# Optimization experiments

Measured on AMD Instinct MI355X. Metric: run time of the kernel, lower is better.

The kernel has to match this reference:

```python
import jax, jax.numpy as jnp
import numpy as np

B, S, H = 16, 2048, 1024

def setup_inputs() -> dict:
    key = jax.random.key(0)
    k1, k2, k3, k4 = jax.random.split(key, 4)
    x = jax.random.normal(k1, (B, S, H), dtype=jnp.float32)
    # nn.Linear weights, stored as (out, in); y = x @ W.T
    scale = 1.0 / np.sqrt(H)
    W_q = jax.random.uniform(k2, (H, H), jnp.float32, -scale, scale)
    W_k = jax.random.uniform(k3, (H, H), jnp.float32, -scale, scale)
    W_v = jax.random.uniform(k4, (H, H), jnp.float32, -scale, scale)
    return {"x": x, "W_q": W_q, "W_k": W_k, "W_v": W_v}

def reference(x, W_q, W_k, W_v):
    # x: (B,S,H); W_*: (H,H) torch Linear layout (out,in)
    Q = jnp.einsum('bsh,oh->bso', x, W_q)
    K = jnp.einsum('bsh,oh->bso', x, W_k)
    V = jnp.einsum('bsh,oh->bso', x, W_v)
    scale = jnp.asarray(x.shape[-1] ** 0.5, dtype=x.dtype)
    energy = jnp.einsum('bqd,bkd->bqk', Q, K) / scale      # (B,S,S)
    attn = jax.nn.softmax(energy, axis=-1)                  # (B,S,S)
    attended = jnp.einsum('bqk,bkd->bqd', attn, V)          # (B,S,H)
    context = attended.mean(axis=1)                         # (B,H)
    attn_weights = attn.mean(axis=1)                        # (B,S)
    return (context, attn_weights)
```

## Files before the change

kernel.cpp:

```cpp
#include <hip/hip_runtime.h>
#include <hip/hip_bf16.h>
#include <stdint.h>

#define BB 16
#define SS 2048
#define HH 1024

using bf16 = __hip_bfloat16;
typedef __attribute__((ext_vector_type(8))) short short8;
typedef __attribute__((ext_vector_type(4))) float f32x4;

typedef unsigned int __attribute__((address_space(1))) as1_uint;
typedef unsigned int __attribute__((address_space(3))) as3_uint;

static constexpr size_t WS_XB   = 0;
static constexpr size_t WS_G    = 67108864;
static constexpr size_t WS_P    = 134217728;
static constexpr size_t WS_WQT  = 134217728;
static constexpr size_t WS_WKT  = 136314880;
static constexpr size_t WS_MT   = 138412032;
static constexpr size_t WS_LSUM = 201326592;
static constexpr size_t WS_T    = 201457664;
static constexpr size_t WS_NEED = 201523200;

__device__ __forceinline__ void async_copy16(bf16* lds_dst, const bf16* gsrc) {
    __builtin_amdgcn_global_load_lds((const as1_uint*)gsrc, (as3_uint*)lds_dst, 16, 0, 0);
}

__device__ __forceinline__ float bf2f(unsigned short u) {
    union { unsigned i; float f; } v; v.i = (unsigned)u << 16; return v.f;
}

__device__ __forceinline__ unsigned char f32_to_e4m3(float x) {
#if __has_builtin(__builtin_amdgcn_cvt_pk_fp8_f32)
    return (unsigned char)(__builtin_amdgcn_cvt_pk_fp8_f32(x, x, 0, false) & 0xff);
#else
    if (x >= 0.015625f) {
        union { float f; unsigned u; } v; v.f = x;
        int e = (v.u >> 23) & 0xff;
        unsigned m = v.u & 0x7fffff;
        unsigned mant = m >> 20;
        unsigned rem = m & 0xfffff;
        mant += (rem > 0x80000u) || (rem == 0x80000u && (mant & 1));
        int oe = e - 120;
        if (mant == 8) { mant = 0; oe += 1; }
        return (unsigned char)((oe << 3) | mant);
    }
    int code = (int)rintf(x * 512.0f);
    return (unsigned char)code;
#endif
}

__device__ __forceinline__ float e4m3_to_f32(unsigned char b) {
#if __has_builtin(__builtin_amdgcn_cvt_pk_f32_fp8)
    auto v = __builtin_amdgcn_cvt_pk_f32_fp8((int)b, false);
    return v[0];
#else
    int e = (b >> 3) & 15, m = b & 7;
    if (e) { union { unsigned u; float f; } v; v.u = ((unsigned)(e + 120) << 23) | ((unsigned)m << 20); return v.f; }
    return (float)m * 0.001953125f;
#endif
}

__global__ __launch_bounds__(256) void cast_x_kernel(const float* __restrict__ x,
                                                     bf16* __restrict__ xb, int n4) {
    int stride = gridDim.x * blockDim.x;
    for (int i = blockIdx.x * blockDim.x + threadIdx.x; i < n4; i += stride) {
        float4 v = reinterpret_cast<const float4*>(x)[i];
        union { bf16 h[4]; uint2 u; } p;
        p.h[0] = __float2bfloat16(v.x); p.h[1] = __float2bfloat16(v.y);
        p.h[2] = __float2bfloat16(v.z); p.h[3] = __float2bfloat16(v.w);
        reinterpret_cast<uint2*>(xb)[i] = p.u;
    }
}

__global__ __launch_bounds__(256) void transpose_w_kernel(const float* __restrict__ wq,
                                                          const float* __restrict__ wk,
                                                          bf16* __restrict__ wqT,
                                                          bf16* __restrict__ wkT) {
    __shared__ float tile[64][65];
    const float* src = blockIdx.z ? wk : wq;
    bf16* dst = blockIdx.z ? wkT : wqT;
    const int o0 = blockIdx.y * 64, i0 = blockIdx.x * 64;
    const int tr = threadIdx.x >> 4;
    const int tc = (threadIdx.x & 15) * 4;
#pragma unroll
    for (int k = 0; k < 4; ++k) {
        float4 v = *reinterpret_cast<const float4*>(src + (size_t)(o0 + tr + k * 16) * 1024 + i0 + tc);
        tile[tr + k * 16][tc + 0] = v.x; tile[tr + k * 16][tc + 1] = v.y;
        tile[tr + k * 16][tc + 2] = v.z; tile[tr + k * 16][tc + 3] = v.w;
    }
    __syncthreads();
#pragma unroll
    for (int k = 0; k < 4; ++k) {
        int ri = tr + k * 16;
        union { bf16 h[4]; uint2 u; } p;
#pragma unroll
        for (int j = 0; j < 4; ++j) p.h[j] = __float2bfloat16(tile[tc + j][ri]);
        *reinterpret_cast<uint2*>(dst + (size_t)(i0 + ri) * 1024 + o0 + tc) = p.u;
    }
}

__global__ __launch_bounds__(256) void gemm_mt64(const bf16* __restrict__ wkT,
                                                 const bf16* __restrict__ wqT,
                                                 bf16* __restrict__ Mt) {
    __shared__ bf16 As[64 * 64], Bs[64 * 64];
    f32x4 acc[2][2];
#pragma unroll
    for (int m = 0; m < 2; ++m)
#pragma unroll
        for (int n = 0; n < 2; ++n) { acc[m][n][0]=0.f; acc[m][n][1]=0.f; acc[m][n][2]=0.f; acc[m][n][3]=0.f; }
    const int tid = threadIdx.x, wid = tid >> 6, lane = tid & 63;
    const int wm = wid >> 1, wn = wid & 1;
    const int srow = lane >> 3, scol = (lane & 7) * 8;
    const bf16* Ab = wkT + (size_t)blockIdx.y * 64 * 1024;
    const bf16* Bb = wqT + (size_t)blockIdx.x * 64 * 1024;
    for (int kt = 0; kt < 1024; kt += 64) {
#pragma unroll
        for (int i = 0; i < 2; ++i) {
            int row0 = i * 32 + wid * 8;
            async_copy16(As + row0 * 64, Ab + (size_t)(row0 + srow) * 1024 + kt + scol);
            async_copy16(Bs + row0 * 64, Bb + (size_t)(row0 + srow) * 1024 + kt + scol);
        }
        __syncthreads();
#pragma unroll
        for (int kk = 0; kk < 2; ++kk) {
            short8 a[2], b[2];
#pragma unroll
            for (int m = 0; m < 2; ++m)
                a[m] = *reinterpret_cast<const short8*>(
                    As + (wm * 32 + m * 16 + (lane & 15)) * 64 + kk * 32 + (lane >> 4) * 8);
#pragma unroll
            for (int n = 0; n < 2; ++n)
                b[n] = *reinterpret_cast<const short8*>(
                    Bs + (wn * 32 + n * 16 + (lane & 15)) * 64 + kk * 32 + (lane >> 4) * 8);
#pragma unroll
            for (int m = 0; m < 2; ++m)
#pragma unroll
                for (int n = 0; n < 2; ++n)
                    acc[m][n] = __builtin_amdgcn_mfma_f32_16x16x32_bf16(a[m], b[n], acc[m][n], 0, 0, 0);
        }
        __syncthreads();
    }
    const int row0 = blockIdx.y * 64 + wm * 32 + ((lane >> 4) << 2);
    const int col0 = blockIdx.x * 64 + wn * 32 + (lane & 15);
#pragma unroll
    for (int m = 0; m < 2; ++m)
#pragma unroll
        for (int n = 0; n < 2; ++n)
#pragma unroll
            for (int r = 0; r < 4; ++r)
                Mt[(size_t)(row0 + m * 16 + r) * 1024 + col0 + n * 16] =
                    __float2bfloat16(acc[m][n][r] * 0.03125f);
}

static constexpr int NT256 = 16;

__device__ __forceinline__ void gemm256_mainloop(const bf16* __restrict__ Ag,
                                                 const bf16* __restrict__ Bg,
                                                 char* lds, f32x4 acc[8][4]) {
    const int tid = threadIdx.x;
    const int lane = tid & 63;
    const int wid = tid >> 6;
    const int wm = wid >> 2;
    const int wn = wid & 3;

#pragma unroll
    for (int m = 0; m < 8; ++m)
#pragma unroll
        for (int n = 0; n < 4; ++n) { acc[m][n][0]=0.f; acc[m][n][1]=0.f; acc[m][n][2]=0.f; acc[m][n][3]=0.f; }

    char* A0 = lds;            char* B0 = lds + 32768;
    char* A1 = lds + 65536;    char* B1 = lds + 98304;

    int soA[2], soB[2];
    {
#pragma unroll
        for (int i = 0; i < 2; ++i) {
            int beta = (i * 512 + tid) * 16;
            int rho  = beta >> 7;
            int cs   = (beta & 127) ^ ((rho & 7) << 4);
            soA[i] = ((rho >> 6) * 128 + (rho & 63)) * 1024 + (cs >> 1);
            soB[i] = ((rho >> 5) * 64  + (rho & 31)) * 1024 + (cs >> 1);
        }
    }
    const int dstw = wid * 1024;

    int roA[4], roB[2];
    {
        const int swz = (lane & 7) << 4;
        const int colb = (lane >> 4) * 16;
#pragma unroll
        for (int mi = 0; mi < 4; ++mi) {
            int row = wm * 64 + mi * 16 + (lane & 15);
            roA[mi] = (row * 128 + colb) ^ swz;
        }
#pragma unroll
        for (int ni = 0; ni < 2; ++ni) {
            int row = wn * 32 + ni * 16 + (lane & 15);
            roB[ni] = (row * 128 + colb) ^ swz;
        }
    }

#define STAGE_A256(buf, q, kt)                                                        \
    {                                                                                 \
        async_copy16((bf16*)((buf) + (q) * 16384 + dstw),                             \
                     Ag + soA[0] + (q) * 65536 + (kt) * 64);                          \
        async_copy16((bf16*)((buf) + (q) * 16384 + 8192 + dstw),                      \
                     Ag + soA[1] + (q) * 65536 + (kt) * 64);                          \
    }
#define STAGE_B256(buf, q, kt)                                                        \
    {                                                                                 \
        async_copy16((bf16*)((buf) + (q) * 16384 + dstw),                             \
                     Bg + soB[0] + (q) * 32768 + (kt) * 64);                          \
        async_copy16((bf16*)((buf) + (q) * 16384 + 8192 + dstw),                      \
                     Bg + soB[1] + (q) * 32768 + (kt) * 64);                          \
    }

    STAGE_A256(A0, 0, 0); STAGE_A256(A0, 1, 0);
    STAGE_B256(B0, 0, 0); STAGE_B256(B0, 1, 0);
    STAGE_A256(A1, 0, 1); STAGE_B256(B1, 0, 1);
    asm volatile("s_waitcnt vmcnt(4)" ::: "memory");
    __builtin_amdgcn_s_barrier();

    short8 a[4][2], b0[2][2], b1[2][2];

#pragma unroll 1
    for (int t = 0; t < NT256; ++t) {
        char* As  = (t & 1) ? A1 : A0;
        char* Bs  = (t & 1) ? B1 : B0;
        char* Aso = (t & 1) ? A0 : A1;
        char* Bso = (t & 1) ? B0 : B1;

#pragma unroll
        for (int ni = 0; ni < 2; ++ni) {
            b0[ni][0] = *reinterpret_cast<const short8*>(Bs + roB[ni]);
            b0[ni][1] = *reinterpret_cast<const short8*>(Bs + (roB[ni] ^ 64));
        }
#pragma unroll
        for (int mi = 0; mi < 4; ++mi) {
            a[mi][0] = *reinterpret_cast<const short8*>(As + roA[mi]);
            a[mi][1] = *reinterpret_cast<const short8*>(As + (roA[mi] ^ 64));
        }
#pragma unroll
        for (int ni = 0; ni < 2; ++ni) {
            b1[ni][0] = *reinterpret_cast<const short8*>(Bs + (roB[ni] + 16384));
            b1[ni][1] = *reinterpret_cast<const short8*>(Bs + ((roB[ni] ^ 64) + 16384));
        }
        if (t + 1 < NT256) { STAGE_A256(Aso, 1, t + 1); STAGE_B256(Bso, 1, t + 1); }
        __builtin_amdgcn_s_setprio(1);
#pragma unroll
        for (int mi = 0; mi < 4; ++mi)
#pragma unroll
            for (int ni = 0; ni < 2; ++ni)
#pragma unroll
                for (int kk = 0; kk < 2; ++kk)
                    acc[mi][ni] = __builtin_amdgcn_mfma_f32_16x16x32_bf16(
                        a[mi][kk], b0[ni][kk], acc[mi][ni], 0, 0, 0);
#pragma unroll
        for (int mi = 0; mi < 4; ++mi)
#pragma unroll
            for (int ni = 0; ni < 2; ++ni)
#pragma unroll
                for (int kk = 0; kk < 2; ++kk)
                    acc[mi][2 + ni] = __builtin_amdgcn_mfma_f32_16x16x32_bf16(
                        a[mi][kk], b1[ni][kk], acc[mi][2 + ni], 0, 0, 0);
        __builtin_amdgcn_s_setprio(0);
        __builtin_amdgcn_sched_barrier(0);
        __builtin_amdgcn_s_barrier();

        if (t + 2 < NT256) { STAGE_A256(As, 0, t + 2); STAGE_B256(Bs, 0, t + 2); }
#pragma unroll
        for (int mi = 0; mi < 4; ++mi) {
            a[mi][0] = *reinterpret_cast<const short8*>(As + (roA[mi] + 16384));
            a[mi][1] = *reinterpret_cast<const short8*>(As + ((roA[mi] ^ 64) + 16384));
        }
        __builtin_amdgcn_s_setprio(1);
#pragma unroll
        for (int mi = 0; mi < 4; ++mi)
#pragma unroll
            for (int ni = 0; ni < 2; ++ni)
#pragma unroll
                for (int kk = 0; kk < 2; ++kk)
                    acc[4 + mi][2 + ni] = __builtin_amdgcn_mfma_f32_16x16x32_bf16(
                        a[mi][kk], b1[ni][kk], acc[4 + mi][2 + ni], 0, 0, 0);
#pragma unroll
        for (int mi = 0; mi < 4; ++mi)
#pragma unroll
            for (int ni = 0; ni < 2; ++ni)
#pragma unroll
                for (int kk = 0; kk < 2; ++kk)
                    acc[4 + mi][ni] = __builtin_amdgcn_mfma_f32_16x16x32_bf16(
                        a[mi][kk], b0[ni][kk], acc[4 + mi][ni], 0, 0, 0);
        __builtin_amdgcn_s_setprio(0);
        __builtin_amdgcn_sched_barrier(0);
        if (t + 2 < NT256) asm volatile("s_waitcnt vmcnt(4)" ::: "memory");
        else               asm volatile("s_waitcnt vmcnt(0)" ::: "memory");
        __builtin_amdgcn_s_barrier();
    }
#undef STAGE_A256
#undef STAGE_B256
}

__global__ __launch_bounds__(512, 2) void gemm_g256(const bf16* __restrict__ xb,
                                                    const bf16* __restrict__ Mt,
                                                    bf16* __restrict__ G) {
    extern __shared__ char lds[];
    f32x4 acc[8][4];
    const int bx = blockIdx.x, by = blockIdx.y;
    gemm256_mainloop(xb + (size_t)by * 256 * 1024, Mt + (size_t)bx * 256 * 1024, lds, acc);
    const int lane = threadIdx.x & 63, wid = threadIdx.x >> 6;
    const int wm = wid >> 2, wn = wid & 3;
    const int row0 = by * 256 + wm * 128 + ((lane >> 4) << 2);
    const int col0 = bx * 256 + wn * 64 + (lane & 15);
#pragma unroll
    for (int mi = 0; mi < 8; ++mi)
#pragma unroll
        for (int ni = 0; ni < 4; ++ni)
#pragma unroll
            for (int r = 0; r < 4; ++r)
                G[(size_t)(row0 + mi * 16 + r) * 1024 + col0 + ni * 16] =
                    __float2bfloat16(acc[mi][ni][r]);
}

__global__ __launch_bounds__(512, 2) void energy_fused256(const bf16* __restrict__ G,
                                                          const bf16* __restrict__ xb,
                                                          unsigned char* __restrict__ P,
                                                          float* __restrict__ lsum) {
    extern __shared__ char lds[];
    f32x4 acc[8][4];
    const int bx = blockIdx.x, by = blockIdx.y, bz = blockIdx.z;
    gemm256_mainloop(G + (size_t)(bz * 2048 + by * 256) * 1024,
                     xb + (size_t)(bz * 2048 + bx * 256) * 1024, lds, acc);
    const int lane = threadIdx.x & 63, wid = threadIdx.x >> 6;
    const int wm = wid >> 2, wn = wid & 3;
    const int q0 = bz * 2048 + by * 256 + wm * 128 + ((lane >> 4) << 2);
    const int k0 = bx * 256 + wn * 64 + (lane & 15);
#pragma unroll
    for (int mi = 0; mi < 8; ++mi) {
        float s[4] = {0.f, 0.f, 0.f, 0.f};
#pragma unroll
        for (int ni = 0; ni < 4; ++ni)
#pragma unroll
            for (int r = 0; r < 4; ++r) {
                float e = __expf(acc[mi][ni][r]);
                unsigned char c = f32_to_e4m3(e);
                P[(size_t)(q0 + mi * 16 + r) * 2048 + k0 + ni * 16] = c;
                s[r] += e4m3_to_f32(c);
            }
#pragma unroll
        for (int off = 1; off < 16; off <<= 1)
#pragma unroll
            for (int r = 0; r < 4; ++r) s[r] += __shfl_xor(s[r], off, 64);
        if ((lane & 15) == 0) {
#pragma unroll
            for (int r = 0; r < 4; ++r) atomicAdd(&lsum[q0 + mi * 16 + r], s[r]);
        }
    }
}

__global__ __launch_bounds__(256) void colsum_kernel(const unsigned char* __restrict__ P,
                                                     const float* __restrict__ lsum,
                                                     float* __restrict__ aw) {
    const int b = blockIdx.y, qc = blockIdx.x, t = threadIdx.x;
    float acc[8] = {0.f, 0.f, 0.f, 0.f, 0.f, 0.f, 0.f, 0.f};
    const unsigned char* base = P + (size_t)(b * 2048 + qc * 128) * 2048 + t * 8;
    const float* ls = lsum + b * 2048 + qc * 128;
    for (int q = 0; q < 128; ++q) {
        float w = 1.0f / ls[q];
        uint2 v = *reinterpret_cast<const uint2*>(base + (size_t)q * 2048);
#if __has_builtin(__builtin_amdgcn_cvt_pk_f32_fp8)
        auto p0 = __builtin_amdgcn_cvt_pk_f32_fp8((int)v.x, false);
        auto p1 = __builtin_amdgcn_cvt_pk_f32_fp8((int)v.x, true);
        auto p2 = __builtin_amdgcn_cvt_pk_f32_fp8((int)v.y, false);
        auto p3 = __builtin_amdgcn_cvt_pk_f32_fp8((int)v.y, true);
        acc[0] += p0[0] * w; acc[1] += p0[1] * w;
        acc[2] += p1[0] * w; acc[3] += p1[1] * w;
        acc[4] += p2[0] * w; acc[5] += p2[1] * w;
        acc[6] += p3[0] * w; acc[7] += p3[1] * w;
#else
        unsigned char by8[8];
        *reinterpret_cast<uint2*>(by8) = v;
#pragma unroll
        for (int j = 0; j < 8; ++j) acc[j] += e4m3_to_f32(by8[j]) * w;
#endif
    }
#pragma unroll
    for (int j = 0; j < 8; ++j)
        atomicAdd(&aw[b * 2048 + t * 8 + j], acc[j] * (1.0f / 2048.0f));
}

__global__ __launch_bounds__(256) void av_x_kernel(const float* __restrict__ aw,
                                                   const bf16* __restrict__ xb,
                                                   float* __restrict__ t) {
    const int b = blockIdx.y;
    const int kc = blockIdx.x;
    const int tid = threadIdx.x;
    float4 acc = {0.f, 0.f, 0.f, 0.f};
    const int k0 = kc * 128;
#pragma unroll 4
    for (int k = k0; k < k0 + 128; ++k) {
        float w = aw[b * 2048 + k];
        uint2 v = *reinterpret_cast<const uint2*>(xb + (size_t)(b * 2048 + k) * 1024 + tid * 4);
        acc.x += w * bf2f((unsigned short)(v.x & 0xffff));
        acc.y += w * bf2f((unsigned short)(v.x >> 16));
        acc.z += w * bf2f((unsigned short)(v.y & 0xffff));
        acc.w += w * bf2f((unsigned short)(v.y >> 16));
    }
    float* tp = t + b * 1024 + tid * 4;
    atomicAdd(tp + 0, acc.x); atomicAdd(tp + 1, acc.y);
    atomicAdd(tp + 2, acc.z); atomicAdd(tp + 3, acc.w);
}

__global__ __launch_bounds__(256) void ctx_gemv_kernel(const float* __restrict__ t,
                                                       const float* __restrict__ wv,
                                                       float* __restrict__ ctx) {
    const int b = blockIdx.y;
    const int wid = threadIdx.x >> 6, lane = threadIdx.x & 63;
    const int o = blockIdx.x * 4 + wid;
    const float4* t4 = reinterpret_cast<const float4*>(t + b * 1024);
    const float4* w4 = reinterpret_cast<const float4*>(wv + (size_t)o * 1024);
    float s = 0.f;
#pragma unroll
    for (int j = lane; j < 256; j += 64) {
        float4 a = t4[j], w = w4[j];
        s += a.x * w.x + a.y * w.y + a.z * w.z + a.w * w.w;
    }
#pragma unroll
    for (int off = 1; off < 64; off <<= 1) s += __shfl_xor(s, off, 64);
    if (lane == 0) ctx[b * 1024 + o] = s;
}

__global__ void ws_too_small_kernel(float* out) {
    if (threadIdx.x == 0 && blockIdx.x == 0) out[0] = 12345.0f;
}

extern "C" void kernel_launch(void* const* d_in, const int* in_sizes, int n_in,
                              void* d_out, int out_size, void* d_ws, size_t ws_size,
                              hipStream_t stream) {
    const float* x  = (const float*)d_in[0];
    const float* wq = (const float*)d_in[1];
    const float* wk = (const float*)d_in[2];
    const float* wv = (const float*)d_in[3];
    float* out = (float*)d_out;
    float* ctx = out;
    float* aw  = out + 16384;

    if (ws_size < WS_NEED) {
        hipMemsetAsync(d_out, 0, (size_t)out_size * sizeof(float), stream);
        ws_too_small_kernel<<<1, 64, 0, stream>>>(out);
        return;
    }

    char* ws = (char*)d_ws;
    bf16* xb   = (bf16*)(ws + WS_XB);
    bf16* G    = (bf16*)(ws + WS_G);
    unsigned char* P = (unsigned char*)(ws + WS_P);
    bf16* wqT  = (bf16*)(ws + WS_WQT);
    bf16* wkT  = (bf16*)(ws + WS_WKT);
    bf16* Mt   = (bf16*)(ws + WS_MT);
    float* lsum = (float*)(ws + WS_LSUM);
    float* t    = (float*)(ws + WS_T);

    hipMemsetAsync(d_out, 0, (size_t)out_size * sizeof(float), stream);
    hipMemsetAsync(lsum, 0, 131072 + 65536, stream);

    cast_x_kernel<<<2048, 256, 0, stream>>>(x, xb, (BB * SS * HH) / 4);
    transpose_w_kernel<<<dim3(16, 16, 2), 256, 0, stream>>>(wq, wk, wqT, wkT);

    gemm_mt64<<<dim3(16, 16), 256, 0, stream>>>(wkT, wqT, Mt);
    gemm_g256<<<dim3(4, 128), 512, 131072, stream>>>(xb, Mt, G);

    energy_fused256<<<dim3(8, 8, 16), 512, 131072, stream>>>(G, xb, P, lsum);
    colsum_kernel<<<dim3(16, 16), 256, 0, stream>>>(P, lsum, aw);

    av_x_kernel<<<dim3(16, 16), 256, 0, stream>>>(aw, xb, t);
    ctx_gemv_kernel<<<dim3(256, 16), 256, 0, stream>>>(t, wv, ctx);
}
```

Measured before the change: 317.0 us.

## Store fp8 probabilities transposed with packed 4-byte writes; rewrite colsum per key row

The energy kernel now writes the fp8 exp matrix in transposed (key-major) layout, packing four consecutive query values into one 32-bit store instead of four scattered byte stores. The column-sum kernel is restructured so each wavefront reduces one contiguous key row with a shuffle reduction, which removes the float atomics into the output. exp is also switched to a hardware exp2-based path. Each PT store still has a 2048-byte stride between lanes, so the write pattern is only partially coalesced. The new colsum does a division per element instead of one reciprocal per row.

```diff
diff --git a/kernel.cpp b/kernel.cpp
--- a/kernel.cpp
+++ b/kernel.cpp
@@ -29,6 +29,14 @@
 
 __device__ __forceinline__ float bf2f(unsigned short u) {
     union { unsigned i; float f; } v; v.i = (unsigned)u << 16; return v.f;
+}
+
+__device__ __forceinline__ float fast_exp(float x) {
+#if __has_builtin(__builtin_amdgcn_exp2f)
+    return __builtin_amdgcn_exp2f(x * 1.4426950408889634f);
+#else
+    return __expf(x);
+#endif
 }
 
 __device__ __forceinline__ unsigned char f32_to_e4m3(float x) {
@@ -325,7 +333,7 @@
 
 __global__ __launch_bounds__(512, 2) void energy_fused256(const bf16* __restrict__ G,
                                                           const bf16* __restrict__ xb,
-                                                          unsigned char* __restrict__ P,
+                                                          unsigned char* __restrict__ PT,
                                                           float* __restrict__ lsum) {
     extern __shared__ char lds[];
     f32x4 acc[8][4];
@@ -334,60 +342,58 @@
                      xb + (size_t)(bz * 2048 + bx * 256) * 1024, lds, acc);
     const int lane = threadIdx.x & 63, wid = threadIdx.x >> 6;
     const int wm = wid >> 2, wn = wid & 3;
-    const int q0 = bz * 2048 + by * 256 + wm * 128 + ((lane >> 4) << 2);
-    const int k0 = bx * 256 + wn * 64 + (lane & 15);
+    const int q0g = bz * 2048 + by * 256 + wm * 128 + ((lane >> 4) << 2);
+    const int ql0 = by * 256 + wm * 128 + ((lane >> 4) << 2);
+    const int kl0 = bx * 256 + wn * 64 + (lane & 15);
 #pragma unroll
     for (int mi = 0; mi < 8; ++mi) {
         float s[4] = {0.f, 0.f, 0.f, 0.f};
 #pragma unroll
-        for (int ni = 0; ni < 4; ++ni)
+        for (int ni = 0; ni < 4; ++ni) {
+            unsigned pack = 0;
 #pragma unroll
             for (int r = 0; r < 4; ++r) {
-                float e = __expf(acc[mi][ni][r]);
+                float e = fast_exp(acc[mi][ni][r]);
                 unsigned char c = f32_to_e4m3(e);
-                P[(size_t)(q0 + mi * 16 + r) * 2048 + k0 + ni * 16] = c;
+                pack |= (unsigned)c << (8 * r);
                 s[r] += e4m3_to_f32(c);
             }
+            *reinterpret_cast<unsigned*>(
+                PT + ((size_t)(bz * 2048 + kl0 + ni * 16) * 2048) + ql0 + mi * 16) = pack;
+        }
 #pragma unroll
         for (int off = 1; off < 16; off <<= 1)
 #pragma unroll
             for (int r = 0; r < 4; ++r) s[r] += __shfl_xor(s[r], off, 64);
         if ((lane & 15) == 0) {
 #pragma unroll
-            for (int r = 0; r < 4; ++r) atomicAdd(&lsum[q0 + mi * 16 + r], s[r]);
-        }
-    }
-}
-
-__global__ __launch_bounds__(256) void colsum_kernel(const unsigned char* __restrict__ P,
+            for (int r = 0; r < 4; ++r) atomicAdd(&lsum[q0g + mi * 16 + r], s[r]);
+        }
+    }
+}
+
+__global__ __launch_bounds__(256) void colsum_kernel(const unsigned char* __restrict__ PT,
                                                      const float* __restrict__ lsum,
                                                      float* __restrict__ aw) {
-    const int b = blockIdx.y, qc = blockIdx.x, t = threadIdx.x;
-    float acc[8] = {0.f, 0.f, 0.f, 0.f, 0.f, 0.f, 0.f, 0.f};
-    const unsigned char* base = P + (size_t)(b * 2048 + qc * 128) * 2048 + t * 8;
-    const float* ls = lsum + b * 2048 + qc * 128;
-    for (int q = 0; q < 128; ++q) {
-        float w = 1.0f / ls[q];
-        uint2 v = *reinterpret_cast<const uint2*>(base + (size_t)q * 2048);
-#if __has_builtin(__builtin_amdgcn_cvt_pk_f32_fp8)
-        auto p0 = __builtin_amdgcn_cvt_pk_f32_fp8((int)v.x, false);
-        auto p1 = __builtin_amdgcn_cvt_pk_f32_fp8((int)v.x, true);
-        auto p2 = __builtin_amdgcn_cvt_pk_f32_fp8((int)v.y, false);
-        auto p3 = __builtin_amdgcn_cvt_pk_f32_fp8((int)v.y, true);
-        acc[0] += p0[0] * w; acc[1] += p0[1] * w;
-        acc[2] += p1[0] * w; acc[3] += p1[1] * w;
-        acc[4] += p2[0] * w; acc[5] += p2[1] * w;
-        acc[6] += p3[0] * w; acc[7] += p3[1] * w;
-#else
-        unsigned char by8[8];
-        *reinterpret_cast<uint2*>(by8) = v;
-#pragma unroll
-        for (int j = 0; j < 8; ++j) acc[j] += e4m3_to_f32(by8[j]) * w;
-#endif
-    }
-#pragma unroll
-    for (int j = 0; j < 8; ++j)
-        atomicAdd(&aw[b * 2048 + t * 8 + j], acc[j] * (1.0f / 2048.0f));
+    const int b = blockIdx.y;
+    const int wid = threadIdx.x >> 6, lane = threadIdx.x & 63;
+    const int k = blockIdx.x * 4 + wid;
+    const unsigned char* row = PT + (size_t)(b * 2048 + k) * 2048;
+    const float* ls = lsum + b * 2048;
+    float s = 0.f;
+#pragma unroll
+    for (int it = 0; it < 8; ++it) {
+        int q = (it * 64 + lane) * 4;
+        unsigned v = *reinterpret_cast<const unsigned*>(row + q);
+        float4 l4 = *reinterpret_cast<const float4*>(ls + q);
+        s += e4m3_to_f32((unsigned char)(v & 0xff)) / l4.x;
+        s += e4m3_to_f32((unsigned char)((v >> 8) & 0xff)) / l4.y;
+        s += e4m3_to_f32((unsigned char)((v >> 16) & 0xff)) / l4.z;
+        s += e4m3_to_f32((unsigned char)((v >> 24) & 0xff)) / l4.w;
+    }
+#pragma unroll
+    for (int off = 1; off < 64; off <<= 1) s += __shfl_xor(s, off, 64);
+    if (lane == 0) aw[b * 2048 + k] = s * (1.0f / 2048.0f);
 }
 
 __global__ __launch_bounds__(256) void av_x_kernel(const float* __restrict__ aw,
@@ -455,7 +461,7 @@
     char* ws = (char*)d_ws;
     bf16* xb   = (bf16*)(ws + WS_XB);
     bf16* G    = (bf16*)(ws + WS_G);
-    unsigned char* P = (unsigned char*)(ws + WS_P);
+    unsigned char* PT = (unsigned char*)(ws + WS_P);
     bf16* wqT  = (bf16*)(ws + WS_WQT);
     bf16* wkT  = (bf16*)(ws + WS_WKT);
     bf16* Mt   = (bf16*)(ws + WS_MT);
@@ -471,8 +477,8 @@
     gemm_mt64<<<dim3(16, 16), 256, 0, stream>>>(wkT, wqT, Mt);
     gemm_g256<<<dim3(4, 128), 512, 131072, stream>>>(xb, Mt, G);
 
-    energy_fused256<<<dim3(8, 8, 16), 512, 131072, stream>>>(G, xb, P, lsum);
-    colsum_kernel<<<dim3(16, 16), 256, 0, stream>>>(P, lsum, aw);
+    energy_fused256<<<dim3(8, 8, 16), 512, 131072, stream>>>(G, xb, PT, lsum);
+    colsum_kernel<<<dim3(512, 16), 256, 0, stream>>>(PT, lsum, aw);
 
     av_x_kernel<<<dim3(16, 16), 256, 0, stream>>>(aw, xb, t);
     ctx_gemv_kernel<<<dim3(256, 16), 256, 0, stream>>>(t, wv, ctx);
```

Result: slower. 327.8 us (+3.4%).
